# Kernel tuning notes

Hardware: AMD Instinct MI355X
Metric: run time of the kernel (lower is better)

Reference implementation:

```python
import jax, jax.numpy as jnp
import numpy as np

DIM_ATTN = 64
DIM_H = DIM_ATTN // 2


def _xavier(key, shape, fan_in, fan_out, dtype=jnp.float32):
    limit = float(np.sqrt(6.0 / (fan_in + fan_out)))
    return jax.random.uniform(key, shape, dtype, -limit, limit)


def setup_inputs() -> dict:
    key = jax.random.key(0)
    k_cell, k_drug, k_wq, k_wk, k_b, k_a = jax.random.split(key, 6)
    B, Nc, Nd = 8, 1024, 1024
    cell = jax.random.normal(k_cell, (B, Nc, DIM_ATTN), jnp.float32)
    drug = jax.random.normal(k_drug, (B, Nd, DIM_ATTN), jnp.float32)
    w_q = _xavier(k_wq, (DIM_ATTN, DIM_H), DIM_ATTN, DIM_H)
    w_k = _xavier(k_wk, (DIM_ATTN, DIM_H), DIM_ATTN, DIM_H)
    # bias/a are xavier-init'd as [dim_h, 1] views: fan_in=dim_h, fan_out=1
    bias = _xavier(k_b, (DIM_H,), DIM_H, 1)
    a = _xavier(k_a, (DIM_H,), DIM_H, 1)
    return {"cell": cell, "drug": drug, "w_q": w_q, "w_k": w_k, "bias": bias, "a": a}


def reference(cell, drug, w_q, w_k, bias, a):
    # cell: [B, Nc, D], drug: [B, Nd, D]
    cell_attn = cell @ w_k  # [B, Nc, H]
    drug_attn = drug @ w_q  # [B, Nd, H]
    # broadcast additive co-attention: [B, Nc, Nd, H]
    e = cell_attn[:, :, None, :] + drug_attn[:, None, :, :] + bias
    attentions = jnp.tanh(e) @ a  # [B, Nc, Nd]
    return attentions
```

## Files before the change

kernel.cpp:

```cpp
#include <hip/hip_runtime.h>
#include <hip/hip_bf16.h>


#define BB    8
#define NC    1024
#define ND    1024
#define DD    64
#define HH    32
#define CHUNK 16
#define C2    2.885390081777927f
#define EPS16 1.52587890625e-05f
#define SCALE (-3.0517578125e-05f)

__global__ __launch_bounds__(256) void proj_cell_kernel(
    const float* __restrict__ cell, const float* __restrict__ w_k,
    const float* __restrict__ bias, float* __restrict__ pu)
{
    int tid = threadIdx.x;
    int h = tid & 31;
    int i = blockIdx.x * 8 + (tid >> 5);
    int b = blockIdx.y;
    const float* crow = cell + ((size_t)(b * NC + i)) * DD;
    float s = bias[h];
    #pragma unroll
    for (int d = 0; d < DD; ++d)
        s = fmaf(crow[d], w_k[d * HH + h], s);
    pu[((size_t)(b * NC + i)) * HH + h] = exp2f(fmaf(C2, s, -16.0f));
}

__global__ __launch_bounds__(256) void proj_drug_kernel(
    const float* __restrict__ drug, const float* __restrict__ w_q,
    float* __restrict__ pv)
{
    __shared__ float sd[64][65];
    int tid = threadIdx.x;
    int b = blockIdx.y;
    int j0 = blockIdx.x * 64;
    const float* dbase = drug + ((size_t)(b * ND + j0)) * DD;
    #pragma unroll
    for (int k = 0; k < 16; ++k) {
        int idx = k * 256 + tid;
        sd[idx >> 6][idx & 63] = dbase[idx];
    }
    __syncthreads();
    int jl = tid & 63;
    int hg = tid >> 6;
    #pragma unroll
    for (int hh = 0; hh < 8; ++hh) {
        int h = hg * 8 + hh;
        float s = 0.f;
        #pragma unroll
        for (int d = 0; d < DD; ++d)
            s = fmaf(sd[jl][d], w_q[d * HH + h], s);
        pv[((size_t)(b * HH + h)) * ND + j0 + jl] = exp2f(C2 * s);
    }
}

__global__ __launch_bounds__(256) void coattn_kernel(
    const float* __restrict__ pu, const float* __restrict__ pv,
    const float* __restrict__ a, float* __restrict__ out)
{
    __shared__ float spu[CHUNK * HH];
    int tid = threadIdx.x;
    int j  = blockIdx.x * 256 + tid;
    int b  = blockIdx.z;
    int i0 = blockIdx.y * CHUNK;

    {
        const float* src = pu + ((size_t)(b * NC + i0)) * HH;
        reinterpret_cast<float2*>(spu)[tid] =
            reinterpret_cast<const float2*>(src)[tid];
    }

    float pvr[HH];
    #pragma unroll
    for (int h = 0; h < HH; ++h)
        pvr[h] = pv[((size_t)(b * HH + h)) * ND + j];

    float av[HH];
    #pragma unroll
    for (int h = 0; h < HH; ++h)
        av[h] = a[h];
    float A = 0.f;
    #pragma unroll
    for (int h = 0; h < HH; ++h)
        A += av[h];

    __syncthreads();

    float* orow = out + ((size_t)(b * NC + i0)) * ND + j;

    #pragma unroll
    for (int ii = 0; ii < CHUNK; ++ii) {
        float pur[HH];
        #pragma unroll
        for (int h4 = 0; h4 < HH / 4; ++h4) {
            float4 t = reinterpret_cast<const float4*>(spu + ii * HH)[h4];
            pur[4 * h4 + 0] = t.x;
            pur[4 * h4 + 1] = t.y;
            pur[4 * h4 + 2] = t.z;
            pur[4 * h4 + 3] = t.w;
        }

        float acc0 = 0.f, acc1 = 0.f;
        #pragma unroll
        for (int q = 0; q < HH / 4; ++q) {
            float u = fmaf(pur[4 * q + 0], pvr[4 * q + 0], EPS16);
            float v = fmaf(pur[4 * q + 1], pvr[4 * q + 1], EPS16);
            float w = fmaf(pur[4 * q + 2], pvr[4 * q + 2], EPS16);
            float z = fmaf(pur[4 * q + 3], pvr[4 * q + 3], EPS16);
            float n01 = fmaf(av[4 * q + 1], u, av[4 * q + 0] * v);
            float d01 = u * v;
            float n23 = fmaf(av[4 * q + 3], w, av[4 * q + 2] * z);
            float d23 = w * z;
            float den = d01 * d23;
            float num = fmaf(n23, d01, n01 * d23);
            float r   = __builtin_amdgcn_rcpf(den);
            if (q & 1) acc1 = fmaf(num, r, acc1);
            else       acc0 = fmaf(num, r, acc0);
        }
        orow[ii * ND] = fmaf(acc0 + acc1, SCALE, A);
    }
}

extern "C" void kernel_launch(void* const* d_in, const int* in_sizes, int n_in,
                              void* d_out, int out_size, void* d_ws, size_t ws_size,
                              hipStream_t stream) {
    const float* cell = (const float*)d_in[0];
    const float* drug = (const float*)d_in[1];
    const float* w_q  = (const float*)d_in[2];
    const float* w_k  = (const float*)d_in[3];
    const float* bias = (const float*)d_in[4];
    const float* a    = (const float*)d_in[5];
    float* out = (float*)d_out;

    float* pu = (float*)d_ws;
    float* pv = pu + (size_t)BB * NC * HH;

    proj_cell_kernel<<<dim3(NC / 8, BB), 256, 0, stream>>>(cell, w_k, bias, pu);
    proj_drug_kernel<<<dim3(ND / 64, BB), 256, 0, stream>>>(drug, w_q, pv);
    coattn_kernel<<<dim3(ND / 256, NC / CHUNK, BB), 256, 0, stream>>>(pu, pv, a, out);
}
```

Measured before the change: 121.3 us.

## Compute four output columns per thread with float4 pv loads and stores

Each thread now handles four adjacent j columns, loading pv as float4 and writing float4 outputs, so each shared-memory read of pu is reused across four columns. CHUNK is halved to 8 rows per block and the grid x dimension shrinks to one block per batch row-chunk. This raises register use (128 pv values per thread), which may lower occupancy, in exchange for fewer LDS reads and wider global memory transactions.

```diff
diff --git a/kernel.cpp b/kernel.cpp
--- a/kernel.cpp
+++ b/kernel.cpp
@@ -7,7 +7,7 @@
 #define ND    1024
 #define DD    64
 #define HH    32
-#define CHUNK 16
+#define CHUNK 8
 #define C2    2.885390081777927f
 #define EPS16 1.52587890625e-05f
 #define SCALE (-3.0517578125e-05f)
@@ -62,20 +62,18 @@
 {
     __shared__ float spu[CHUNK * HH];
     int tid = threadIdx.x;
-    int j  = blockIdx.x * 256 + tid;
-    int b  = blockIdx.z;
-    int i0 = blockIdx.y * CHUNK;
+    int j4  = blockIdx.x * 1024 + tid * 4;
+    int b   = blockIdx.z;
+    int i0  = blockIdx.y * CHUNK;
 
-    {
-        const float* src = pu + ((size_t)(b * NC + i0)) * HH;
-        reinterpret_cast<float2*>(spu)[tid] =
-            reinterpret_cast<const float2*>(src)[tid];
+    spu[tid] = pu[((size_t)(b * NC + i0)) * HH + tid];
+
+    float pvr[HH][4];
+    #pragma unroll
+    for (int h = 0; h < HH; ++h) {
+        float4 t = *reinterpret_cast<const float4*>(&pv[((size_t)(b * HH + h)) * ND + j4]);
+        pvr[h][0] = t.x; pvr[h][1] = t.y; pvr[h][2] = t.z; pvr[h][3] = t.w;
     }
-
-    float pvr[HH];
-    #pragma unroll
-    for (int h = 0; h < HH; ++h)
-        pvr[h] = pv[((size_t)(b * HH + h)) * ND + j];
 
     float av[HH];
     #pragma unroll
@@ -88,38 +86,43 @@
 
     __syncthreads();
 
-    float* orow = out + ((size_t)(b * NC + i0)) * ND + j;
+    float* orow = out + ((size_t)(b * NC + i0)) * ND + j4;
 
     #pragma unroll
     for (int ii = 0; ii < CHUNK; ++ii) {
-        float pur[HH];
-        #pragma unroll
-        for (int h4 = 0; h4 < HH / 4; ++h4) {
-            float4 t = reinterpret_cast<const float4*>(spu + ii * HH)[h4];
-            pur[4 * h4 + 0] = t.x;
-            pur[4 * h4 + 1] = t.y;
-            pur[4 * h4 + 2] = t.z;
-            pur[4 * h4 + 3] = t.w;
-        }
-
-        float acc0 = 0.f, acc1 = 0.f;
+        float acc0[4] = {0.f, 0.f, 0.f, 0.f};
+        float acc1[4] = {0.f, 0.f, 0.f, 0.f};
         #pragma unroll
         for (int q = 0; q < HH / 4; ++q) {
-            float u = fmaf(pur[4 * q + 0], pvr[4 * q + 0], EPS16);
-            float v = fmaf(pur[4 * q + 1], pvr[4 * q + 1], EPS16);
-            float w = fmaf(pur[4 * q + 2], pvr[4 * q + 2], EPS16);
-            float z = fmaf(pur[4 * q + 3], pvr[4 * q + 3], EPS16);
-            float n01 = fmaf(av[4 * q + 1], u, av[4 * q + 0] * v);
-            float d01 = u * v;
-            float n23 = fmaf(av[4 * q + 3], w, av[4 * q + 2] * z);
-            float d23 = w * z;
-            float den = d01 * d23;
-            float num = fmaf(n23, d01, n01 * d23);
-            float r   = __builtin_amdgcn_rcpf(den);
-            if (q & 1) acc1 = fmaf(num, r, acc1);
-            else       acc0 = fmaf(num, r, acc0);
+            float4 pqv = reinterpret_cast<const float4*>(spu + ii * HH)[q];
+            float pq[4];
+            pq[0] = pqv.x; pq[1] = pqv.y; pq[2] = pqv.z; pq[3] = pqv.w;
+            float s0 = av[4 * q + 0], s1 = av[4 * q + 1];
+            float s2 = av[4 * q + 2], s3 = av[4 * q + 3];
+
+            #pragma unroll
+            for (int s = 0; s < 4; ++s) {
+                float u = fmaf(pq[0], pvr[4 * q + 0][s], EPS16);
+                float v = fmaf(pq[1], pvr[4 * q + 1][s], EPS16);
+                float w = fmaf(pq[2], pvr[4 * q + 2][s], EPS16);
+                float z = fmaf(pq[3], pvr[4 * q + 3][s], EPS16);
+                float n01 = fmaf(s1, u, s0 * v);
+                float d01 = u * v;
+                float n23 = fmaf(s3, w, s2 * z);
+                float d23 = w * z;
+                float den = d01 * d23;
+                float num = fmaf(n23, d01, n01 * d23);
+                float r   = __builtin_amdgcn_rcpf(den);
+                if (q & 1) acc1[s] = fmaf(num, r, acc1[s]);
+                else       acc0[s] = fmaf(num, r, acc0[s]);
+            }
         }
-        orow[ii * ND] = fmaf(acc0 + acc1, SCALE, A);
+        float4 res;
+        res.x = fmaf(acc0[0] + acc1[0], SCALE, A);
+        res.y = fmaf(acc0[1] + acc1[1], SCALE, A);
+        res.z = fmaf(acc0[2] + acc1[2], SCALE, A);
+        res.w = fmaf(acc0[3] + acc1[3], SCALE, A);
+        *reinterpret_cast<float4*>(&orow[(size_t)ii * ND]) = res;
     }
 }
 
@@ -139,5 +142,5 @@
 
     proj_cell_kernel<<<dim3(NC / 8, BB), 256, 0, stream>>>(cell, w_k, bias, pu);
     proj_drug_kernel<<<dim3(ND / 64, BB), 256, 0, stream>>>(drug, w_q, pv);
-    coattn_kernel<<<dim3(ND / 256, NC / CHUNK, BB), 256, 0, stream>>>(pu, pv, a, out);
+    coattn_kernel<<<dim3(ND / 1024, NC / CHUNK, BB), 256, 0, stream>>>(pu, pv, a, out);
 }
```

Result: no change. 119.5 us (-1.5%).
